# Kernel optimization log

Measured on AMD Instinct MI355X. Metric: run time of the kernel, lower is better.

The kernel has to match this reference:

```python
import jax, jax.numpy as jnp
import numpy as np

VOCAB, ENC, DEC, ATT, EMB = 10000, 2048, 512, 512, 512
B, P, L = 64, 196, 20


def setup_inputs() -> dict:
    key = jax.random.key(0)
    ks = jax.random.split(key, 24)
    s = lambda k, shape, fan: jax.random.normal(k, shape, jnp.float32) / np.sqrt(fan)
    inp = {
        "img_features": jax.random.normal(ks[0], (B, P, ENC), jnp.float32),
        "captions": jax.random.randint(ks[1], (B, L), 0, VOCAB),
        # init-state projections
        "W_init_h": s(ks[2], (DEC, ENC), ENC), "b_init_h": jnp.zeros((DEC,), jnp.float32),
        "W_init_c": s(ks[3], (DEC, ENC), ENC), "b_init_c": jnp.zeros((DEC,), jnp.float32),
        # attention
        "W_dec": s(ks[4], (ATT, DEC), DEC), "b_dec": jnp.zeros((ATT,), jnp.float32),
        "W_enc": s(ks[5], (ATT, ENC), ENC), "b_enc": jnp.zeros((ATT,), jnp.float32),
        "W_fin": s(ks[6], (1, ATT), ATT), "b_fin": jnp.zeros((1,), jnp.float32),
        # gate + output + embedding
        "W_gate": s(ks[7], (ENC, DEC), DEC), "b_gate": jnp.zeros((ENC,), jnp.float32),
        "W_out": s(ks[8], (VOCAB, DEC), DEC), "b_out": jnp.zeros((VOCAB,), jnp.float32),
        "emb": s(ks[9], (VOCAB, EMB), EMB),
        # LSTMCell (PyTorch gate order: i, f, g, o)
        "W_ih": s(ks[10], (4 * DEC, EMB + ENC), EMB + ENC), "b_ih": jnp.zeros((4 * DEC,), jnp.float32),
        "W_hh": s(ks[11], (4 * DEC, DEC), DEC), "b_hh": jnp.zeros((4 * DEC,), jnp.float32),
    }
    return inp


def _decode(img_features, captions, W_init_h, b_init_h, W_init_c, b_init_c,
            W_dec, b_dec, W_enc, b_enc, W_fin, b_fin,
            W_gate, b_gate, W_out, b_out, emb, W_ih, W_hh, b_ih, b_hh):
    # lengths are uniform (padded tensor), so sort/restore are identity and
    # batch_size_t == B at every step.
    avg = img_features.mean(axis=1)                              # [B,ENC]
    h0 = jnp.tanh(avg @ W_init_h.T + b_init_h)                   # [B,DEC]
    c0 = jnp.tanh(avg @ W_init_c.T + b_init_c)
    enc_proj = img_features @ W_enc.T + b_enc                    # [B,P,ATT] (loop-invariant)
    emb_seq = emb[captions[:, :-1]]                              # [B,T,EMB], T = L-1

    def step(carry, e_t):
        h, c = carry
        U_h = h @ W_dec.T + b_dec                                # [B,ATT]
        att = jnp.tanh(enc_proj + U_h[:, None, :])               # [B,P,ATT]
        e = (att @ W_fin.T + b_fin)[..., 0]                      # [B,P]
        alpha = jax.nn.softmax(e, axis=1)
        context = jnp.einsum('bpe,bp->be', img_features, alpha)  # [B,ENC]
        gate = jax.nn.sigmoid(h @ W_gate.T + b_gate)             # [B,ENC]
        x = jnp.concatenate([e_t, gate * context], axis=1)       # [B,EMB+ENC]
        gates = x @ W_ih.T + b_ih + h @ W_hh.T + b_hh            # [B,4*DEC]
        i, f, g, o = jnp.split(gates, 4, axis=1)
        c_new = jax.nn.sigmoid(f) * c + jax.nn.sigmoid(i) * jnp.tanh(g)
        h_new = jax.nn.sigmoid(o) * jnp.tanh(c_new)
        out = h_new @ W_out.T + b_out                            # [B,VOCAB] (dropout=eval identity)
        return (h_new, c_new), (out, alpha)

    _, (preds, alphas) = jax.lax.scan(step, (h0, c0), jnp.swapaxes(emb_seq, 0, 1))
    return jnp.swapaxes(preds, 0, 1), jnp.swapaxes(alphas, 0, 1)  # [B,T,VOCAB], [B,T,P]


def reference(img_features, captions, W_init_h, b_init_h, W_init_c, b_init_c,
              W_dec, b_dec, W_enc, b_enc, W_fin, b_fin,
              W_gate, b_gate, W_out, b_out, emb, W_ih, W_hh, b_ih, b_hh):
    return _decode(img_features, captions, W_init_h, b_init_h, W_init_c, b_init_c,
                   W_dec, b_dec, W_enc, b_enc, W_fin, b_fin,
                   W_gate, b_gate, W_out, b_out, emb, W_ih, W_hh, b_ih, b_hh)
```

## Files before the change

kernel.cpp:

```cpp
#include <hip/hip_runtime.h>
#include <hip/hip_bf16.h>

typedef unsigned short u16;
typedef unsigned int   u32;

#define BB    64
#define PP    196
#define ENC   2048
#define DEC   512
#define ATT   512
#define EMB   512
#define VOCAB 10000
#define VPAD  10048
#define TT    19
#define LCAP  20
#define XDIM  3072
#define LDSTR 40
#define LD64  72

typedef __bf16 bf16x8 __attribute__((ext_vector_type(8)));
typedef float  f32x4  __attribute__((ext_vector_type(4)));

__device__ __forceinline__ float bf2f(u16 u) {
  union { float f; u32 i; } v; v.i = ((u32)u) << 16; return v.f;
}
__device__ __forceinline__ u16 f2bf(float f) {
  u32 x = __float_as_uint(f);
  u32 r = (x + 0x7FFFu + ((x >> 16) & 1u)) >> 16;
  return (u16)r;
}
__device__ __forceinline__ u32 pack2(float a, float b) {
  return (u32)f2bf(a) | ((u32)f2bf(b) << 16);
}
__device__ __forceinline__ float wred_sum(float v) {
  #pragma unroll
  for (int off = 32; off > 0; off >>= 1) v += __shfl_xor(v, off, 64);
  return v;
}
__device__ __forceinline__ float wred_max(float v) {
  #pragma unroll
  for (int off = 32; off > 0; off >>= 1) v = fmaxf(v, __shfl_xor(v, off, 64));
  return v;
}
__device__ __forceinline__ float tanh_fast(float x) {
  return 1.f - 2.f / (__expf(2.f * x) + 1.f);
}
__device__ __forceinline__ float sigm(float x) {
  return 1.f / (1.f + __expf(-x));
}

__global__ __launch_bounds__(256) void k_cvt_simple(u16* __restrict__ dst,
    const float* __restrict__ src, int n4) {
  int stride = gridDim.x * blockDim.x;
  for (int i = blockIdx.x * blockDim.x + threadIdx.x; i < n4; i += stride) {
    float4 v = ((const float4*)src)[i];
    ((uint2*)dst)[i] = make_uint2(pack2(v.x, v.y), pack2(v.z, v.w));
  }
}

__global__ __launch_bounds__(256) void k_cvt_pad(u16* __restrict__ dst,
    const float* __restrict__ src) {
  int total = VPAD * (DEC / 2);
  int stride = gridDim.x * blockDim.x;
  for (int i = blockIdx.x * blockDim.x + threadIdx.x; i < total; i += stride) {
    int row = i >> 8, c2 = i & 255;
    u32 v = 0;
    if (row < VOCAB) {
      float2 f = ((const float2*)src)[(size_t)row * 256 + c2];
      v = pack2(f.x, f.y);
    }
    ((u32*)dst)[i] = v;
  }
}

__global__ __launch_bounds__(256) void k_cvt_comb(u16* __restrict__ dst,
    const float* __restrict__ Wih, const float* __restrict__ Whh) {
  int j = blockIdx.x;
  for (int t = threadIdx.x; t < 768; t += 256) {
    int col = t * 4;
    float4 v = (col < 2560)
        ? ((const float4*)(Wih + (size_t)j * 2560))[t]
        : ((const float4*)(Whh + (size_t)j * 512))[(col - 2560) >> 2];
    ((uint2*)(dst + (size_t)j * XDIM))[t] = make_uint2(pack2(v.x, v.y), pack2(v.z, v.w));
  }
}

__global__ __launch_bounds__(256) void k_avg(const float* __restrict__ img,
    u16* __restrict__ avgb) {
  int b = blockIdx.x;
  int col = blockIdx.y * 256 + threadIdx.x;
  const float* base = img + (size_t)b * PP * ENC + col;
  float s = 0.f;
  for (int p = 0; p < PP; ++p) s += base[(size_t)p * ENC];
  avgb[b * ENC + col] = f2bf(s * (1.f / PP));
}

__global__ __launch_bounds__(256) void k_init_mfma(const u16* __restrict__ avgb,
    const u16* __restrict__ Winitb, const float* __restrict__ bh,
    const float* __restrict__ bc, u16* __restrict__ h, float* __restrict__ c) {
  __shared__ __align__(16) u16 As[2 * 64 * LD64];
  __shared__ __align__(16) u16 Bs[2 * 64 * LD64];
  int n0 = blockIdx.x * 64;
  int tid = threadIdx.x, wv = tid >> 6, lane = tid & 63;
  int wm = wv >> 1, wn = wv & 1;
  int fr = lane & 15, kg = (lane >> 4) * 8, rq = lane >> 4;
  int r0 = tid >> 3, kc0 = (tid & 7) * 8;
  int r1 = (tid + 256) >> 3, kc1 = ((tid + 256) & 7) * 8;
  uint4 pa0 = *(const uint4*)&avgb[(size_t)r0 * ENC + kc0];
  uint4 pa1 = *(const uint4*)&avgb[(size_t)r1 * ENC + kc1];
  uint4 pb0 = *(const uint4*)&Winitb[(size_t)(n0 + r0) * ENC + kc0];
  uint4 pb1 = *(const uint4*)&Winitb[(size_t)(n0 + r1) * ENC + kc1];
  f32x4 acc[2][2] = {};
  const int NK = ENC / 64;
  for (int kt = 0; kt < NK; ++kt) {
    u16* as = As + (kt & 1) * (64 * LD64);
    u16* bs = Bs + (kt & 1) * (64 * LD64);
    *(uint4*)&as[r0 * LD64 + kc0] = pa0;
    *(uint4*)&as[r1 * LD64 + kc1] = pa1;
    *(uint4*)&bs[r0 * LD64 + kc0] = pb0;
    *(uint4*)&bs[r1 * LD64 + kc1] = pb1;
    __syncthreads();
    if (kt + 1 < NK) {
      int k0 = (kt + 1) * 64;
      pa0 = *(const uint4*)&avgb[(size_t)r0 * ENC + k0 + kc0];
      pa1 = *(const uint4*)&avgb[(size_t)r1 * ENC + k0 + kc1];
      pb0 = *(const uint4*)&Winitb[(size_t)(n0 + r0) * ENC + k0 + kc0];
      pb1 = *(const uint4*)&Winitb[(size_t)(n0 + r1) * ENC + k0 + kc1];
    }
    #pragma unroll
    for (int ks = 0; ks < 2; ++ks) {
      bf16x8 a0 = *(const bf16x8*)&as[(wm * 32 + fr) * LD64 + ks * 32 + kg];
      bf16x8 a1 = *(const bf16x8*)&as[(wm * 32 + 16 + fr) * LD64 + ks * 32 + kg];
      bf16x8 b0 = *(const bf16x8*)&bs[(wn * 32 + fr) * LD64 + ks * 32 + kg];
      bf16x8 b1 = *(const bf16x8*)&bs[(wn * 32 + 16 + fr) * LD64 + ks * 32 + kg];
      acc[0][0] = __builtin_amdgcn_mfma_f32_16x16x32_bf16(a0, b0, acc[0][0], 0, 0, 0);
      acc[0][1] = __builtin_amdgcn_mfma_f32_16x16x32_bf16(a0, b1, acc[0][1], 0, 0, 0);
      acc[1][0] = __builtin_amdgcn_mfma_f32_16x16x32_bf16(a1, b0, acc[1][0], 0, 0, 0);
      acc[1][1] = __builtin_amdgcn_mfma_f32_16x16x32_bf16(a1, b1, acc[1][1], 0, 0, 0);
    }
  }
  #pragma unroll
  for (int mi = 0; mi < 2; ++mi)
    for (int ni = 0; ni < 2; ++ni)
      #pragma unroll
      for (int r = 0; r < 4; ++r) {
        int m = wm * 32 + mi * 16 + rq * 4 + r;
        int n = n0 + wn * 32 + ni * 16 + fr;
        float v = acc[mi][ni][r];
        if (n < DEC) h[m * DEC + n] = f2bf(tanh_fast(v + bh[n]));
        else         c[m * DEC + (n - DEC)] = tanh_fast(v + bc[n - DEC]);
      }
}

__global__ __launch_bounds__(256) void k_encproj(const float* __restrict__ A,
    const float* __restrict__ Wencf, const float* __restrict__ benc, u16* __restrict__ epj) {
  __shared__ __align__(16) u16 As[128 * LDSTR];
  __shared__ __align__(16) u16 Bs[128 * LDSTR];
  int m0 = blockIdx.x * 128, n0 = blockIdx.y * 128;
  int tid = threadIdx.x, wv = tid >> 6, lane = tid & 63;
  int wm = wv >> 1, wn = wv & 1;
  int fr = lane & 15, kg = (lane >> 4) * 8, rq = lane >> 4;
  f32x4 acc[4][4] = {};
  for (int k0 = 0; k0 < ENC; k0 += 32) {
    __syncthreads();
    #pragma unroll
    for (int i = 0; i < 2; ++i) {
      int id = tid + i * 256;
      int r = id >> 2, kc = id & 3;
      const float* asrc = &A[(size_t)(m0 + r) * ENC + k0 + kc * 8];
      float4 f0 = ((const float4*)asrc)[0];
      float4 f1 = ((const float4*)asrc)[1];
      *(uint4*)(&As[r * LDSTR + kc * 8]) =
          make_uint4(pack2(f0.x, f0.y), pack2(f0.z, f0.w),
                     pack2(f1.x, f1.y), pack2(f1.z, f1.w));
      const float* bsrc = &Wencf[(size_t)(n0 + r) * ENC + k0 + kc * 8];
      float4 g0 = ((const float4*)bsrc)[0];
      float4 g1 = ((const float4*)bsrc)[1];
      *(uint4*)(&Bs[r * LDSTR + kc * 8]) =
          make_uint4(pack2(g0.x, g0.y), pack2(g0.z, g0.w),
                     pack2(g1.x, g1.y), pack2(g1.z, g1.w));
    }
    __syncthreads();
    bf16x8 af[4], bfr[4];
    #pragma unroll
    for (int i = 0; i < 4; ++i) {
      af[i]  = *(const bf16x8*)(&As[(wm * 64 + i * 16 + fr) * LDSTR + kg]);
      bfr[i] = *(const bf16x8*)(&Bs[(wn * 64 + i * 16 + fr) * LDSTR + kg]);
    }
    #pragma unroll
    for (int mi = 0; mi < 4; ++mi)
      #pragma unroll
      for (int ni = 0; ni < 4; ++ni)
        acc[mi][ni] = __builtin_amdgcn_mfma_f32_16x16x32_bf16(af[mi], bfr[ni], acc[mi][ni], 0, 0, 0);
  }
  #pragma unroll
  for (int mi = 0; mi < 4; ++mi)
    for (int ni = 0; ni < 4; ++ni)
      #pragma unroll
      for (int r = 0; r < 4; ++r) {
        int m = m0 + wm * 64 + mi * 16 + rq * 4 + r;
        int n = n0 + wn * 64 + ni * 16 + fr;
        epj[(size_t)m * ATT + n] = f2bf(acc[mi][ni][r] + benc[n]);
      }
}

__global__ __launch_bounds__(256) void k_hcons(const u16* __restrict__ h,
    const u16* __restrict__ Wdecb, const float* __restrict__ bdec,
    const u16* __restrict__ Wgateb, const float* __restrict__ bgate,
    const u16* __restrict__ Woutb, const float* __restrict__ bout,
    float* __restrict__ uh, float* __restrict__ gate,
    float* __restrict__ preds, u16* __restrict__ x, int step) {
  __shared__ __align__(16) u16 As[2 * 64 * LD64];
  __shared__ __align__(16) u16 Bs[2 * 64 * LD64];
  int bid = blockIdx.x;
  int tid = threadIdx.x, wv = tid >> 6, lane = tid & 63;
  int wm = wv >> 1, wn = wv & 1;
  int fr = lane & 15, kg = (lane >> 4) * 8, rq = lane >> 4;

  if (bid == 0) {
    for (int i = tid; i < 16384; i += 256) {
      int b = i >> 8, jp = (i & 255) * 2;
      *(u32*)(&x[(size_t)b * XDIM + 2560 + jp]) = *(const u32*)(&h[b * DEC + jp]);
    }
  }

  int role, nt; const u16* Wsrc;
  if (bid < 8)       { role = 0; nt = bid;      Wsrc = Wdecb;  }
  else if (bid < 40) { role = 1; nt = bid - 8;  Wsrc = Wgateb; }
  else               { role = 2; nt = bid - 40; Wsrc = Woutb;  }
  int n0 = nt * 64;

  int r0 = tid >> 3, kc0 = (tid & 7) * 8;
  int r1 = (tid + 256) >> 3, kc1 = ((tid + 256) & 7) * 8;
  uint4 pa0 = *(const uint4*)&h[(size_t)r0 * DEC + kc0];
  uint4 pa1 = *(const uint4*)&h[(size_t)r1 * DEC + kc1];
  uint4 pb0 = *(const uint4*)&Wsrc[(size_t)(n0 + r0) * DEC + kc0];
  uint4 pb1 = *(const uint4*)&Wsrc[(size_t)(n0 + r1) * DEC + kc1];
  f32x4 acc[2][2] = {};
  const int NK = DEC / 64;
  for (int kt = 0; kt < NK; ++kt) {
    u16* as = As + (kt & 1) * (64 * LD64);
    u16* bs = Bs + (kt & 1) * (64 * LD64);
    *(uint4*)&as[r0 * LD64 + kc0] = pa0;
    *(uint4*)&as[r1 * LD64 + kc1] = pa1;
    *(uint4*)&bs[r0 * LD64 + kc0] = pb0;
    *(uint4*)&bs[r1 * LD64 + kc1] = pb1;
    __syncthreads();
    if (kt + 1 < NK) {
      int k0 = (kt + 1) * 64;
      pa0 = *(const uint4*)&h[(size_t)r0 * DEC + k0 + kc0];
      pa1 = *(const uint4*)&h[(size_t)r1 * DEC + k0 + kc1];
      pb0 = *(const uint4*)&Wsrc[(size_t)(n0 + r0) * DEC + k0 + kc0];
      pb1 = *(const uint4*)&Wsrc[(size_t)(n0 + r1) * DEC + k0 + kc1];
    }
    #pragma unroll
    for (int ks = 0; ks < 2; ++ks) {
      bf16x8 a0 = *(const bf16x8*)&as[(wm * 32 + fr) * LD64 + ks * 32 + kg];
      bf16x8 a1 = *(const bf16x8*)&as[(wm * 32 + 16 + fr) * LD64 + ks * 32 + kg];
      bf16x8 b0 = *(const bf16x8*)&bs[(wn * 32 + fr) * LD64 + ks * 32 + kg];
      bf16x8 b1 = *(const bf16x8*)&bs[(wn * 32 + 16 + fr) * LD64 + ks * 32 + kg];
      acc[0][0] = __builtin_amdgcn_mfma_f32_16x16x32_bf16(a0, b0, acc[0][0], 0, 0, 0);
      acc[0][1] = __builtin_amdgcn_mfma_f32_16x16x32_bf16(a0, b1, acc[0][1], 0, 0, 0);
      acc[1][0] = __builtin_amdgcn_mfma_f32_16x16x32_bf16(a1, b0, acc[1][0], 0, 0, 0);
      acc[1][1] = __builtin_amdgcn_mfma_f32_16x16x32_bf16(a1, b1, acc[1][1], 0, 0, 0);
    }
  }
  #pragma unroll
  for (int mi = 0; mi < 2; ++mi)
    for (int ni = 0; ni < 2; ++ni)
      #pragma unroll
      for (int r = 0; r < 4; ++r) {
        int m = wm * 32 + mi * 16 + rq * 4 + r;
        int n = n0 + wn * 32 + ni * 16 + fr;
        float v = acc[mi][ni][r];
        if (role == 0) {
          uh[m * DEC + n] = v + bdec[n];
        } else if (role == 1) {
          gate[m * ENC + n] = sigm(v + bgate[n]);
        } else if (n < VOCAB) {
          preds[(size_t)m * (TT * VOCAB) + (size_t)step * VOCAB + n] = v + bout[n];
        }
      }
}

__global__ __launch_bounds__(256) void k_escore(const float* __restrict__ uh,
    const u16* __restrict__ epj, const float* __restrict__ wfin, const float* __restrict__ bfin,
    const int* __restrict__ captions, const float* __restrict__ emb,
    float* __restrict__ e_ws, u16* __restrict__ x, int step) {
  __shared__ float s_uh[ATT], s_wf[ATT];
  int b = blockIdx.x, pt = blockIdx.y;
  int tid = threadIdx.x;
  for (int i = tid; i < ATT; i += 256) { s_uh[i] = uh[b * ATT + i]; s_wf[i] = wfin[i]; }
  __syncthreads();
  if (pt == 0) {
    int capv = captions[b * LCAP + step];
    float2 f = ((const float2*)(emb + (size_t)capv * EMB))[tid];
    ((u32*)(x + (size_t)b * XDIM))[tid] = pack2(f.x, f.y);
  }
  int w = tid >> 6, lane = tid & 63;
  float b0 = bfin[0];
  for (int pl = w; pl < 49; pl += 4) {
    int p = pt * 49 + pl;
    const u16* row = epj + (size_t)(b * PP + p) * ATT;
    float acc = 0.f;
    #pragma unroll
    for (int ki = 0; ki < 8; ++ki) {
      int a = lane + ki * 64;
      acc += tanh_fast(bf2f(row[a]) + s_uh[a]) * s_wf[a];
    }
    acc = wred_sum(acc);
    if (lane == 0) e_ws[b * PP + p] = acc + b0;
  }
}

template <int SRC>
__global__ __launch_bounds__(256) void k_ctx(const float* __restrict__ e_ws,
    const float* __restrict__ gate, const u16* __restrict__ imgb,
    const float* __restrict__ imgf,
    u16* __restrict__ x, float* __restrict__ alphas, int step) {
  __shared__ float s_a[PP];
  int b = blockIdx.x, et = blockIdx.y;
  int tid = threadIdx.x;
  if (tid < PP) s_a[tid] = e_ws[b * PP + tid];
  __syncthreads();
  if (tid < 64) {
    float v0 = s_a[tid], v1 = s_a[tid + 64], v2 = s_a[tid + 128];
    float v3 = (tid + 192 < PP) ? s_a[tid + 192] : -1e30f;
    float m = wred_max(fmaxf(fmaxf(v0, v1), fmaxf(v2, v3)));
    float e0 = __expf(v0 - m), e1 = __expf(v1 - m), e2 = __expf(v2 - m);
    float e3 = (tid + 192 < PP) ? __expf(v3 - m) : 0.f;
    float inv = 1.f / wred_sum(e0 + e1 + e2 + e3);
    s_a[tid] = e0 * inv; s_a[tid + 64] = e1 * inv; s_a[tid + 128] = e2 * inv;
    if (tid + 192 < PP) s_a[tid + 192] = e3 * inv;
  }
  __syncthreads();
  if (et == 0 && tid < PP)
    alphas[(size_t)b * (TT * PP) + (size_t)step * PP + tid] = s_a[tid];
  int e0i = et * 512 + tid * 2;
  float c0 = 0.f, c1 = 0.f;
  if (SRC == 0) {
    const u16* ib = imgb + (size_t)b * PP * ENC + e0i;
    for (int p = 0; p < PP; ++p) {
      u32 v = *(const u32*)(ib + (size_t)p * ENC);
      float ap = s_a[p];
      c0 += ap * bf2f((u16)(v & 0xFFFF));
      c1 += ap * bf2f((u16)(v >> 16));
    }
  } else {
    const float* ib = imgf + (size_t)b * PP * ENC + e0i;
    for (int p = 0; p < PP; ++p) {
      float2 v = *(const float2*)(ib + (size_t)p * ENC);
      float ap = s_a[p];
      c0 += ap * v.x;
      c1 += ap * v.y;
    }
  }
  float g0 = gate[b * ENC + e0i], g1 = gate[b * ENC + e0i + 1];
  *(u32*)(&x[(size_t)b * XDIM + 512 + e0i]) = pack2(c0 * g0, c1 * g1);
}

__global__ __launch_bounds__(256) void k_lstm_part(const u16* __restrict__ x,
    const u16* __restrict__ Wcomb, float* __restrict__ pbuf) {
  __shared__ __align__(16) u16 As[2 * 64 * LD64];
  __shared__ __align__(16) u16 Bs[2 * 64 * LD64];
  int jt = blockIdx.x, ksp = blockIdx.y;
  int kbase = ksp * 768;
  int tid = threadIdx.x, wv = tid >> 6, lane = tid & 63;
  int wm = wv >> 1, wn = wv & 1;
  int fr = lane & 15, kg = (lane >> 4) * 8, rq = lane >> 4;
  int r0 = tid >> 3, kc0 = (tid & 7) * 8;
  int r1 = (tid + 256) >> 3, kc1 = ((tid + 256) & 7) * 8;
  int wrow0 = (r0 >> 4) * 512 + jt * 16 + (r0 & 15);
  int wrow1 = (r1 >> 4) * 512 + jt * 16 + (r1 & 15);
  uint4 pa0 = *(const uint4*)&x[(size_t)r0 * XDIM + kbase + kc0];
  uint4 pa1 = *(const uint4*)&x[(size_t)r1 * XDIM + kbase + kc1];
  uint4 pb0 = *(const uint4*)&Wcomb[(size_t)wrow0 * XDIM + kbase + kc0];
  uint4 pb1 = *(const uint4*)&Wcomb[(size_t)wrow1 * XDIM + kbase + kc1];
  f32x4 acc[2][2] = {};
  const int NK = 12;
  for (int kt = 0; kt < NK; ++kt) {
    u16* as = As + (kt & 1) * (64 * LD64);
    u16* bs = Bs + (kt & 1) * (64 * LD64);
    *(uint4*)&as[r0 * LD64 + kc0] = pa0;
    *(uint4*)&as[r1 * LD64 + kc1] = pa1;
    *(uint4*)&bs[r0 * LD64 + kc0] = pb0;
    *(uint4*)&bs[r1 * LD64 + kc1] = pb1;
    __syncthreads();
    if (kt + 1 < NK) {
      int k0 = kbase + (kt + 1) * 64;
      pa0 = *(const uint4*)&x[(size_t)r0 * XDIM + k0 + kc0];
      pa1 = *(const uint4*)&x[(size_t)r1 * XDIM + k0 + kc1];
      pb0 = *(const uint4*)&Wcomb[(size_t)wrow0 * XDIM + k0 + kc0];
      pb1 = *(const uint4*)&Wcomb[(size_t)wrow1 * XDIM + k0 + kc1];
    }
    #pragma unroll
    for (int ks = 0; ks < 2; ++ks) {
      bf16x8 a0 = *(const bf16x8*)&as[(wm * 32 + fr) * LD64 + ks * 32 + kg];
      bf16x8 a1 = *(const bf16x8*)&as[(wm * 32 + 16 + fr) * LD64 + ks * 32 + kg];
      bf16x8 b0 = *(const bf16x8*)&bs[(wn * 32 + fr) * LD64 + ks * 32 + kg];
      bf16x8 b1 = *(const bf16x8*)&bs[(wn * 32 + 16 + fr) * LD64 + ks * 32 + kg];
      acc[0][0] = __builtin_amdgcn_mfma_f32_16x16x32_bf16(a0, b0, acc[0][0], 0, 0, 0);
      acc[0][1] = __builtin_amdgcn_mfma_f32_16x16x32_bf16(a0, b1, acc[0][1], 0, 0, 0);
      acc[1][0] = __builtin_amdgcn_mfma_f32_16x16x32_bf16(a1, b0, acc[1][0], 0, 0, 0);
      acc[1][1] = __builtin_amdgcn_mfma_f32_16x16x32_bf16(a1, b1, acc[1][1], 0, 0, 0);
    }
  }
  float* pout = pbuf + (size_t)(ksp * 32 + jt) * 4096;
  #pragma unroll
  for (int mi = 0; mi < 2; ++mi)
    for (int ni = 0; ni < 2; ++ni)
      #pragma unroll
      for (int r = 0; r < 4; ++r) {
        int m = wm * 32 + mi * 16 + rq * 4 + r;
        int n = wn * 32 + ni * 16 + fr;
        pout[m * 64 + n] = acc[mi][ni][r];
      }
}

__global__ __launch_bounds__(256) void k_lstm_fin(const float* __restrict__ pbuf,
    const float* __restrict__ bih, const float* __restrict__ bhh,
    float* __restrict__ c, u16* __restrict__ h) {
  int jt = blockIdx.x, tid = threadIdx.x;
  #pragma unroll
  for (int ii = 0; ii < 4; ++ii) {
    int idx = tid + ii * 256;
    int bb = idx >> 4, jj = idx & 15;
    int j = jt * 16 + jj;
    float g4[4];
    #pragma unroll
    for (int g = 0; g < 4; ++g) {
      float s = 0.f;
      #pragma unroll
      for (int ks = 0; ks < 4; ++ks)
        s += pbuf[(size_t)(ks * 32 + jt) * 4096 + bb * 64 + g * 16 + jj];
      g4[g] = s;
    }
    float iv = g4[0] + bih[j]        + bhh[j];
    float fv = g4[1] + bih[512 + j]  + bhh[512 + j];
    float gv = g4[2] + bih[1024 + j] + bhh[1024 + j];
    float ov = g4[3] + bih[1536 + j] + bhh[1536 + j];
    float co = c[bb * DEC + j];
    float cn = sigm(fv) * co + sigm(iv) * tanh_fast(gv);
    float hn = sigm(ov) * tanh_fast(cn);
    c[bb * DEC + j] = cn;
    h[bb * DEC + j] = f2bf(hn);
  }
}

extern "C" void kernel_launch(void* const* d_in, const int* in_sizes, int n_in,
                              void* d_out, int out_size, void* d_ws, size_t ws_size,
                              hipStream_t stream) {
  const float* img   = (const float*)d_in[0];
  const int*   cap   = (const int*)  d_in[1];
  const float* Winh  = (const float*)d_in[2];
  const float* binh  = (const float*)d_in[3];
  const float* Winc  = (const float*)d_in[4];
  const float* binc  = (const float*)d_in[5];
  const float* Wdec  = (const float*)d_in[6];
  const float* bdec  = (const float*)d_in[7];
  const float* Wenc  = (const float*)d_in[8];
  const float* benc  = (const float*)d_in[9];
  const float* Wfin  = (const float*)d_in[10];
  const float* bfin  = (const float*)d_in[11];
  const float* Wgate = (const float*)d_in[12];
  const float* bgate = (const float*)d_in[13];
  const float* Wout  = (const float*)d_in[14];
  const float* bout  = (const float*)d_in[15];
  const float* emb   = (const float*)d_in[16];
  const float* Wih   = (const float*)d_in[17];
  const float* bih   = (const float*)d_in[18];
  const float* Whh   = (const float*)d_in[19];
  const float* bhh   = (const float*)d_in[20];

  char* ws = (char*)d_ws;
  u16*   epj    = (u16*)  (ws);
  u16*   Winitb = (u16*)  (ws);
  u16*   avgb   = (u16*)  (ws + 4194304);
  u16*   Wcomb  = (u16*)  (ws + 12845056);
  u16*   Woutb  = (u16*)  (ws + 25427968);
  u16*   Wgateb = (u16*)  (ws + 35717120);
  u16*   Wdecb  = (u16*)  (ws + 37814272);
  float* pbuf   = (float*)(ws + 38338560);
  u16*   h      = (u16*)  (ws + 40435712);
  float* c      = (float*)(ws + 40501248);
  float* e_ws   = (float*)(ws + 40632320);
  u16*   x      = (u16*)  (ws + 40683520);
  float* uh     = (float*)(ws + 41076736);
  float* gate   = (float*)(ws + 41207808);
  u16*   imgb   = (u16*)  (ws + 41732096);
  const bool use_imgb = (ws_size >= 93112320ull);

  float* preds  = (float*)d_out;
  float* alphas = (float*)d_out + (size_t)BB * TT * VOCAB;

  k_cvt_simple<<<512,  256, 0, stream>>>(Winitb,                Winh, 262144);
  k_cvt_simple<<<512,  256, 0, stream>>>(Winitb + 512 * ENC,    Winc, 262144);
  if (use_imgb)
    k_cvt_simple<<<4096, 256, 0, stream>>>(imgb, img, 6422528);
  k_cvt_simple<<<512,  256, 0, stream>>>(Wgateb, Wgate, 262144);
  k_cvt_simple<<<128,  256, 0, stream>>>(Wdecb,  Wdec,  65536);
  k_cvt_pad   <<<2048, 256, 0, stream>>>(Woutb,  Wout);
  k_cvt_comb  <<<2048, 256, 0, stream>>>(Wcomb,  Wih, Whh);

  k_avg<<<dim3(BB, 8), 256, 0, stream>>>(img, avgb);
  k_init_mfma<<<16, 256, 0, stream>>>(avgb, Winitb, binh, binc, h, c);
  k_encproj<<<dim3(98, 4), 256, 0, stream>>>(img, Wenc, benc, epj);
  k_hcons<<<40, 256, 0, stream>>>(h, Wdecb, bdec, Wgateb, bgate, Woutb, bout,
                                  uh, gate, nullptr, x, 0);
  for (int t = 0; t < TT; ++t) {
    k_escore<<<dim3(BB, 4), 256, 0, stream>>>(uh, epj, Wfin, bfin, cap, emb, e_ws, x, t);
    if (use_imgb)
      k_ctx<0><<<dim3(BB, 4), 256, 0, stream>>>(e_ws, gate, imgb, img, x, alphas, t);
    else
      k_ctx<1><<<dim3(BB, 4), 256, 0, stream>>>(e_ws, gate, imgb, img, x, alphas, t);
    k_lstm_part<<<dim3(32, 4), 256, 0, stream>>>(x, Wcomb, pbuf);
    k_lstm_fin<<<32, 256, 0, stream>>>(pbuf, bih, bhh, c, h);
    k_hcons<<<197, 256, 0, stream>>>(h, Wdecb, bdec, Wgateb, bgate, Woutb, bout,
                                     uh, gate, preds, x, t);
  }
}
```

Measured before the change: 1.200 ms.

## Fuse attention score and context kernels, fold LSTM finalize via atomic counter

Merges the per-step score kernel and the softmax/context kernel into one 512-thread block per batch row, keeping scores in shared memory instead of a workspace round trip. The LSTM partial-sum kernel now finishes its own reduction: the last of the four split-K blocks, found with an atomic counter, applies the gate nonlinearities. Together these drop two launches per step. The encoder projection also reads pre-converted bf16 image and weight buffers. The trade-off is fewer blocks per attention launch (64 instead of 256) and threadfence/atomic synchronisation in the LSTM kernel.

```diff
diff --git a/kernel.cpp b/kernel.cpp
--- a/kernel.cpp
+++ b/kernel.cpp
@@ -48,6 +48,8 @@
 __device__ __forceinline__ float sigm(float x) {
   return 1.f / (1.f + __expf(-x));
 }
+
+__global__ void k_zero(u32* __restrict__ p) { p[threadIdx.x] = 0; }
 
 __global__ __launch_bounds__(256) void k_cvt_simple(u16* __restrict__ dst,
     const float* __restrict__ src, int n4) {
@@ -152,8 +154,11 @@
       }
 }
 
-__global__ __launch_bounds__(256) void k_encproj(const float* __restrict__ A,
-    const float* __restrict__ Wencf, const float* __restrict__ benc, u16* __restrict__ epj) {
+template <int SRC>
+__global__ __launch_bounds__(256) void k_encproj(
+    const u16* __restrict__ Ab, const float* __restrict__ Af,
+    const u16* __restrict__ Wb, const float* __restrict__ Wf,
+    const float* __restrict__ benc, u16* __restrict__ epj) {
   __shared__ __align__(16) u16 As[128 * LDSTR];
   __shared__ __align__(16) u16 Bs[128 * LDSTR];
   int m0 = blockIdx.x * 128, n0 = blockIdx.y * 128;
@@ -167,18 +172,23 @@
     for (int i = 0; i < 2; ++i) {
       int id = tid + i * 256;
       int r = id >> 2, kc = id & 3;
-      const float* asrc = &A[(size_t)(m0 + r) * ENC + k0 + kc * 8];
-      float4 f0 = ((const float4*)asrc)[0];
-      float4 f1 = ((const float4*)asrc)[1];
-      *(uint4*)(&As[r * LDSTR + kc * 8]) =
-          make_uint4(pack2(f0.x, f0.y), pack2(f0.z, f0.w),
-                     pack2(f1.x, f1.y), pack2(f1.z, f1.w));
-      const float* bsrc = &Wencf[(size_t)(n0 + r) * ENC + k0 + kc * 8];
-      float4 g0 = ((const float4*)bsrc)[0];
-      float4 g1 = ((const float4*)bsrc)[1];
-      *(uint4*)(&Bs[r * LDSTR + kc * 8]) =
-          make_uint4(pack2(g0.x, g0.y), pack2(g0.z, g0.w),
-                     pack2(g1.x, g1.y), pack2(g1.z, g1.w));
+      if (SRC == 0) {
+        *(uint4*)(&As[r * LDSTR + kc * 8]) = *(const uint4*)(&Ab[(size_t)(m0 + r) * ENC + k0 + kc * 8]);
+        *(uint4*)(&Bs[r * LDSTR + kc * 8]) = *(const uint4*)(&Wb[(size_t)(n0 + r) * ENC + k0 + kc * 8]);
+      } else {
+        const float* asrc = &Af[(size_t)(m0 + r) * ENC + k0 + kc * 8];
+        float4 f0 = ((const float4*)asrc)[0];
+        float4 f1 = ((const float4*)asrc)[1];
+        *(uint4*)(&As[r * LDSTR + kc * 8]) =
+            make_uint4(pack2(f0.x, f0.y), pack2(f0.z, f0.w),
+                       pack2(f1.x, f1.y), pack2(f1.z, f1.w));
+        const float* bsrc = &Wf[(size_t)(n0 + r) * ENC + k0 + kc * 8];
+        float4 g0 = ((const float4*)bsrc)[0];
+        float4 g1 = ((const float4*)bsrc)[1];
+        *(uint4*)(&Bs[r * LDSTR + kc * 8]) =
+            make_uint4(pack2(g0.x, g0.y), pack2(g0.z, g0.w),
+                       pack2(g1.x, g1.y), pack2(g1.z, g1.w));
+      }
     }
     __syncthreads();
     bf16x8 af[4], bfr[4];
@@ -283,24 +293,26 @@
       }
 }
 
-__global__ __launch_bounds__(256) void k_escore(const float* __restrict__ uh,
+template <int SRC>
+__global__ __launch_bounds__(512) void k_att(const float* __restrict__ uh,
     const u16* __restrict__ epj, const float* __restrict__ wfin, const float* __restrict__ bfin,
     const int* __restrict__ captions, const float* __restrict__ emb,
-    float* __restrict__ e_ws, u16* __restrict__ x, int step) {
+    const float* __restrict__ gate, const u16* __restrict__ imgb,
+    const float* __restrict__ imgf,
+    u16* __restrict__ x, float* __restrict__ alphas, int step) {
   __shared__ float s_uh[ATT], s_wf[ATT];
-  int b = blockIdx.x, pt = blockIdx.y;
-  int tid = threadIdx.x;
-  for (int i = tid; i < ATT; i += 256) { s_uh[i] = uh[b * ATT + i]; s_wf[i] = wfin[i]; }
-  __syncthreads();
-  if (pt == 0) {
+  __shared__ float s_e[PP];
+  int b = blockIdx.x;
+  int tid = threadIdx.x, wv = tid >> 6, lane = tid & 63;
+  if (tid < ATT) { s_uh[tid] = uh[b * ATT + tid]; s_wf[tid] = wfin[tid]; }
+  if (tid < 256) {
     int capv = captions[b * LCAP + step];
     float2 f = ((const float2*)(emb + (size_t)capv * EMB))[tid];
     ((u32*)(x + (size_t)b * XDIM))[tid] = pack2(f.x, f.y);
   }
-  int w = tid >> 6, lane = tid & 63;
+  __syncthreads();
   float b0 = bfin[0];
-  for (int pl = w; pl < 49; pl += 4) {
-    int p = pt * 49 + pl;
+  for (int p = wv; p < PP; p += 8) {
     const u16* row = epj + (size_t)(b * PP + p) * ATT;
     float acc = 0.f;
     #pragma unroll
@@ -309,60 +321,55 @@
       acc += tanh_fast(bf2f(row[a]) + s_uh[a]) * s_wf[a];
     }
     acc = wred_sum(acc);
-    if (lane == 0) e_ws[b * PP + p] = acc + b0;
-  }
-}
-
-template <int SRC>
-__global__ __launch_bounds__(256) void k_ctx(const float* __restrict__ e_ws,
-    const float* __restrict__ gate, const u16* __restrict__ imgb,
-    const float* __restrict__ imgf,
-    u16* __restrict__ x, float* __restrict__ alphas, int step) {
-  __shared__ float s_a[PP];
-  int b = blockIdx.x, et = blockIdx.y;
-  int tid = threadIdx.x;
-  if (tid < PP) s_a[tid] = e_ws[b * PP + tid];
+    if (lane == 0) s_e[p] = acc + b0;
+  }
   __syncthreads();
   if (tid < 64) {
-    float v0 = s_a[tid], v1 = s_a[tid + 64], v2 = s_a[tid + 128];
-    float v3 = (tid + 192 < PP) ? s_a[tid + 192] : -1e30f;
+    float v0 = s_e[tid], v1 = s_e[tid + 64], v2 = s_e[tid + 128];
+    float v3 = (tid + 192 < PP) ? s_e[tid + 192] : -1e30f;
     float m = wred_max(fmaxf(fmaxf(v0, v1), fmaxf(v2, v3)));
     float e0 = __expf(v0 - m), e1 = __expf(v1 - m), e2 = __expf(v2 - m);
     float e3 = (tid + 192 < PP) ? __expf(v3 - m) : 0.f;
     float inv = 1.f / wred_sum(e0 + e1 + e2 + e3);
-    s_a[tid] = e0 * inv; s_a[tid + 64] = e1 * inv; s_a[tid + 128] = e2 * inv;
-    if (tid + 192 < PP) s_a[tid + 192] = e3 * inv;
+    s_e[tid] = e0 * inv; s_e[tid + 64] = e1 * inv; s_e[tid + 128] = e2 * inv;
+    if (tid + 192 < PP) s_e[tid + 192] = e3 * inv;
   }
   __syncthreads();
-  if (et == 0 && tid < PP)
-    alphas[(size_t)b * (TT * PP) + (size_t)step * PP + tid] = s_a[tid];
-  int e0i = et * 512 + tid * 2;
-  float c0 = 0.f, c1 = 0.f;
+  if (tid < PP)
+    alphas[(size_t)b * (TT * PP) + (size_t)step * PP + tid] = s_e[tid];
+  int e0i = tid * 4;
+  float c0 = 0.f, c1 = 0.f, c2 = 0.f, c3 = 0.f;
   if (SRC == 0) {
     const u16* ib = imgb + (size_t)b * PP * ENC + e0i;
     for (int p = 0; p < PP; ++p) {
-      u32 v = *(const u32*)(ib + (size_t)p * ENC);
-      float ap = s_a[p];
-      c0 += ap * bf2f((u16)(v & 0xFFFF));
-      c1 += ap * bf2f((u16)(v >> 16));
+      uint2 v = *(const uint2*)(ib + (size_t)p * ENC);
+      float ap = s_e[p];
+      c0 += ap * bf2f((u16)(v.x & 0xFFFF));
+      c1 += ap * bf2f((u16)(v.x >> 16));
+      c2 += ap * bf2f((u16)(v.y & 0xFFFF));
+      c3 += ap * bf2f((u16)(v.y >> 16));
     }
   } else {
     const float* ib = imgf + (size_t)b * PP * ENC + e0i;
     for (int p = 0; p < PP; ++p) {
-      float2 v = *(const float2*)(ib + (size_t)p * ENC);
-      float ap = s_a[p];
-      c0 += ap * v.x;
-      c1 += ap * v.y;
-    }
-  }
-  float g0 = gate[b * ENC + e0i], g1 = gate[b * ENC + e0i + 1];
-  *(u32*)(&x[(size_t)b * XDIM + 512 + e0i]) = pack2(c0 * g0, c1 * g1);
-}
-
-__global__ __launch_bounds__(256) void k_lstm_part(const u16* __restrict__ x,
-    const u16* __restrict__ Wcomb, float* __restrict__ pbuf) {
+      float4 v = *(const float4*)(ib + (size_t)p * ENC);
+      float ap = s_e[p];
+      c0 += ap * v.x; c1 += ap * v.y; c2 += ap * v.z; c3 += ap * v.w;
+    }
+  }
+  float4 g = *(const float4*)(&gate[b * ENC + e0i]);
+  ((uint2*)(x + (size_t)b * XDIM + 512))[tid] =
+      make_uint2(pack2(c0 * g.x, c1 * g.y), pack2(c2 * g.z, c3 * g.w));
+}
+
+__global__ __launch_bounds__(256) void k_lstm(const u16* __restrict__ x,
+    const u16* __restrict__ Wcomb,
+    const float* __restrict__ bih, const float* __restrict__ bhh,
+    float* __restrict__ c, u16* __restrict__ h,
+    float* __restrict__ pbuf, u32* __restrict__ ctr) {
   __shared__ __align__(16) u16 As[2 * 64 * LD64];
   __shared__ __align__(16) u16 Bs[2 * 64 * LD64];
+  __shared__ u32 s_last;
   int jt = blockIdx.x, ksp = blockIdx.y;
   int kbase = ksp * 768;
   int tid = threadIdx.x, wv = tid >> 6, lane = tid & 63;
@@ -415,35 +422,40 @@
         int n = wn * 32 + ni * 16 + fr;
         pout[m * 64 + n] = acc[mi][ni][r];
       }
-}
-
-__global__ __launch_bounds__(256) void k_lstm_fin(const float* __restrict__ pbuf,
-    const float* __restrict__ bih, const float* __restrict__ bhh,
-    float* __restrict__ c, u16* __restrict__ h) {
-  int jt = blockIdx.x, tid = threadIdx.x;
-  #pragma unroll
-  for (int ii = 0; ii < 4; ++ii) {
-    int idx = tid + ii * 256;
-    int bb = idx >> 4, jj = idx & 15;
-    int j = jt * 16 + jj;
-    float g4[4];
-    #pragma unroll
-    for (int g = 0; g < 4; ++g) {
-      float s = 0.f;
+  __threadfence();
+  __syncthreads();
+  if (tid == 0) {
+    u32 old = atomicAdd(&ctr[jt], 1);
+    s_last = (old == 3) ? 1u : 0u;
+  }
+  __syncthreads();
+  if (s_last) {
+    __threadfence();
+    #pragma unroll
+    for (int ii = 0; ii < 4; ++ii) {
+      int idx = tid + ii * 256;
+      int bb = idx >> 4, jj = idx & 15;
+      int j = jt * 16 + jj;
+      float g4[4];
       #pragma unroll
-      for (int ks = 0; ks < 4; ++ks)
-        s += pbuf[(size_t)(ks * 32 + jt) * 4096 + bb * 64 + g * 16 + jj];
-      g4[g] = s;
-    }
-    float iv = g4[0] + bih[j]        + bhh[j];
-    float fv = g4[1] + bih[512 + j]  + bhh[512 + j];
-    float gv = g4[2] + bih[1024 + j] + bhh[1024 + j];
-    float ov = g4[3] + bih[1536 + j] + bhh[1536 + j];
-    float co = c[bb * DEC + j];
-    float cn = sigm(fv) * co + sigm(iv) * tanh_fast(gv);
-    float hn = sigm(ov) * tanh_fast(cn);
-    c[bb * DEC + j] = cn;
-    h[bb * DEC + j] = f2bf(hn);
+      for (int g = 0; g < 4; ++g) {
+        float s = 0.f;
+        #pragma unroll
+        for (int ks = 0; ks < 4; ++ks)
+          s += pbuf[(size_t)(ks * 32 + jt) * 4096 + bb * 64 + g * 16 + jj];
+        g4[g] = s;
+      }
+      float iv = g4[0] + bih[j]        + bhh[j];
+      float fv = g4[1] + bih[512 + j]  + bhh[512 + j];
+      float gv = g4[2] + bih[1024 + j] + bhh[1024 + j];
+      float ov = g4[3] + bih[1536 + j] + bhh[1536 + j];
+      float co = c[bb * DEC + j];
+      float cn = sigm(fv) * co + sigm(iv) * tanh_fast(gv);
+      float hn = sigm(ov) * tanh_fast(cn);
+      c[bb * DEC + j] = cn;
+      h[bb * DEC + j] = f2bf(hn);
+    }
+    if (tid == 0) atomicExch(&ctr[jt], 0);
   }
 }
 
@@ -480,23 +492,27 @@
   u16*   Woutb  = (u16*)  (ws + 25427968);
   u16*   Wgateb = (u16*)  (ws + 35717120);
   u16*   Wdecb  = (u16*)  (ws + 37814272);
-  float* pbuf   = (float*)(ws + 38338560);
-  u16*   h      = (u16*)  (ws + 40435712);
-  float* c      = (float*)(ws + 40501248);
-  float* e_ws   = (float*)(ws + 40632320);
-  u16*   x      = (u16*)  (ws + 40683520);
-  float* uh     = (float*)(ws + 41076736);
-  float* gate   = (float*)(ws + 41207808);
-  u16*   imgb   = (u16*)  (ws + 41732096);
-  const bool use_imgb = (ws_size >= 93112320ull);
+  u16*   Wencb  = (u16*)  (ws + 38338560);
+  float* pbuf   = (float*)(ws + 40435712);
+  u32*   ctr    = (u32*)  (ws + 42532864);
+  u16*   h      = (u16*)  (ws + 42533376);
+  float* c      = (float*)(ws + 42598912);
+  u16*   x      = (u16*)  (ws + 42729984);
+  float* uh     = (float*)(ws + 43123200);
+  float* gate   = (float*)(ws + 43254272);
+  u16*   imgb   = (u16*)  (ws + 43778560);
+  const bool use_imgb = (ws_size >= 95158784ull);
 
   float* preds  = (float*)d_out;
   float* alphas = (float*)d_out + (size_t)BB * TT * VOCAB;
 
-  k_cvt_simple<<<512,  256, 0, stream>>>(Winitb,                Winh, 262144);
-  k_cvt_simple<<<512,  256, 0, stream>>>(Winitb + 512 * ENC,    Winc, 262144);
-  if (use_imgb)
-    k_cvt_simple<<<4096, 256, 0, stream>>>(imgb, img, 6422528);
+  k_zero<<<1, 128, 0, stream>>>(ctr);
+  k_cvt_simple<<<512,  256, 0, stream>>>(Winitb,             Winh, 262144);
+  k_cvt_simple<<<512,  256, 0, stream>>>(Winitb + 512 * ENC, Winc, 262144);
+  if (use_imgb) {
+    k_cvt_simple<<<4096, 256, 0, stream>>>(imgb,  img,  6422528);
+    k_cvt_simple<<<512,  256, 0, stream>>>(Wencb, Wenc, 262144);
+  }
   k_cvt_simple<<<512,  256, 0, stream>>>(Wgateb, Wgate, 262144);
   k_cvt_simple<<<128,  256, 0, stream>>>(Wdecb,  Wdec,  65536);
   k_cvt_pad   <<<2048, 256, 0, stream>>>(Woutb,  Wout);
@@ -504,17 +520,18 @@
 
   k_avg<<<dim3(BB, 8), 256, 0, stream>>>(img, avgb);
   k_init_mfma<<<16, 256, 0, stream>>>(avgb, Winitb, binh, binc, h, c);
-  k_encproj<<<dim3(98, 4), 256, 0, stream>>>(img, Wenc, benc, epj);
+  if (use_imgb)
+    k_encproj<0><<<dim3(98, 4), 256, 0, stream>>>(imgb, img, Wencb, Wenc, benc, epj);
+  else
+    k_encproj<1><<<dim3(98, 4), 256, 0, stream>>>(imgb, img, Wencb, Wenc, benc, epj);
   k_hcons<<<40, 256, 0, stream>>>(h, Wdecb, bdec, Wgateb, bgate, Woutb, bout,
                                   uh, gate, nullptr, x, 0);
   for (int t = 0; t < TT; ++t) {
-    k_escore<<<dim3(BB, 4), 256, 0, stream>>>(uh, epj, Wfin, bfin, cap, emb, e_ws, x, t);
     if (use_imgb)
-      k_ctx<0><<<dim3(BB, 4), 256, 0, stream>>>(e_ws, gate, imgb, img, x, alphas, t);
+      k_att<0><<<BB, 512, 0, stream>>>(uh, epj, Wfin, bfin, cap, emb, gate, imgb, img, x, alphas, t);
     else
-      k_ctx<1><<<dim3(BB, 4), 256, 0, stream>>>(e_ws, gate, imgb, img, x, alphas, t);
-    k_lstm_part<<<dim3(32, 4), 256, 0, stream>>>(x, Wcomb, pbuf);
-    k_lstm_fin<<<32, 256, 0, stream>>>(pbuf, bih, bhh, c, h);
+      k_att<1><<<BB, 512, 0, stream>>>(uh, epj, Wfin, bfin, cap, emb, gate, imgb, img, x, alphas, t);
+    k_lstm<<<dim3(32, 4), 256, 0, stream>>>(x, Wcomb, bih, bhh, c, h, pbuf, ctr);
     k_hcons<<<197, 256, 0, stream>>>(h, Wdecb, bdec, Wgateb, bgate, Woutb, bout,
                                      uh, gate, preds, x, t);
   }
```

Result: slower. 1.671 ms (+39.2%).

## Hoist vocab projection out of recurrence into one batched logits GEMM

Applied to the files above, without the earlier changes.

Each step's bf16 hidden state is saved into a history buffer. The per-step output projection (157 of the 197 blocks of k_hcons) is removed from the recurrent loop and replaced by one 128x128-tile MFMA GEMM over all 19x64 rows after the loop, with W_out padded to a multiple of 128 rows. The trailing k_hcons launch at the last step is also skipped. Separately, the encoder projection now reads pre-converted bf16 image and W_enc instead of converting fp32 on the fly. This adds a W_enc conversion pass and a larger workspace, and the logits GEMM reads padded history rows that are uninitialized but masked on output.

```diff
diff --git a/kernel.cpp b/kernel.cpp
--- a/kernel.cpp
+++ b/kernel.cpp
@@ -11,9 +11,10 @@
 #define ATT   512
 #define EMB   512
 #define VOCAB 10000
-#define VPAD  10048
+#define VPAD2 10112
 #define TT    19
 #define LCAP  20
+#define MALL  1280
 #define XDIM  3072
 #define LDSTR 40
 #define LD64  72
@@ -60,7 +61,7 @@
 
 __global__ __launch_bounds__(256) void k_cvt_pad(u16* __restrict__ dst,
     const float* __restrict__ src) {
-  int total = VPAD * (DEC / 2);
+  int total = VPAD2 * (DEC / 2);
   int stride = gridDim.x * blockDim.x;
   for (int i = blockIdx.x * blockDim.x + threadIdx.x; i < total; i += stride) {
     int row = i >> 8, c2 = i & 255;
@@ -152,8 +153,11 @@
       }
 }
 
-__global__ __launch_bounds__(256) void k_encproj(const float* __restrict__ A,
-    const float* __restrict__ Wencf, const float* __restrict__ benc, u16* __restrict__ epj) {
+template <int SRC>
+__global__ __launch_bounds__(256) void k_encproj(
+    const u16* __restrict__ Ab, const float* __restrict__ Af,
+    const u16* __restrict__ Wb, const float* __restrict__ Wf,
+    const float* __restrict__ benc, u16* __restrict__ epj) {
   __shared__ __align__(16) u16 As[128 * LDSTR];
   __shared__ __align__(16) u16 Bs[128 * LDSTR];
   int m0 = blockIdx.x * 128, n0 = blockIdx.y * 128;
@@ -167,18 +171,23 @@
     for (int i = 0; i < 2; ++i) {
       int id = tid + i * 256;
       int r = id >> 2, kc = id & 3;
-      const float* asrc = &A[(size_t)(m0 + r) * ENC + k0 + kc * 8];
-      float4 f0 = ((const float4*)asrc)[0];
-      float4 f1 = ((const float4*)asrc)[1];
-      *(uint4*)(&As[r * LDSTR + kc * 8]) =
-          make_uint4(pack2(f0.x, f0.y), pack2(f0.z, f0.w),
-                     pack2(f1.x, f1.y), pack2(f1.z, f1.w));
-      const float* bsrc = &Wencf[(size_t)(n0 + r) * ENC + k0 + kc * 8];
-      float4 g0 = ((const float4*)bsrc)[0];
-      float4 g1 = ((const float4*)bsrc)[1];
-      *(uint4*)(&Bs[r * LDSTR + kc * 8]) =
-          make_uint4(pack2(g0.x, g0.y), pack2(g0.z, g0.w),
-                     pack2(g1.x, g1.y), pack2(g1.z, g1.w));
+      if (SRC == 0) {
+        *(uint4*)(&As[r * LDSTR + kc * 8]) = *(const uint4*)(&Ab[(size_t)(m0 + r) * ENC + k0 + kc * 8]);
+        *(uint4*)(&Bs[r * LDSTR + kc * 8]) = *(const uint4*)(&Wb[(size_t)(n0 + r) * ENC + k0 + kc * 8]);
+      } else {
+        const float* asrc = &Af[(size_t)(m0 + r) * ENC + k0 + kc * 8];
+        float4 f0 = ((const float4*)asrc)[0];
+        float4 f1 = ((const float4*)asrc)[1];
+        *(uint4*)(&As[r * LDSTR + kc * 8]) =
+            make_uint4(pack2(f0.x, f0.y), pack2(f0.z, f0.w),
+                       pack2(f1.x, f1.y), pack2(f1.z, f1.w));
+        const float* bsrc = &Wf[(size_t)(n0 + r) * ENC + k0 + kc * 8];
+        float4 g0 = ((const float4*)bsrc)[0];
+        float4 g1 = ((const float4*)bsrc)[1];
+        *(uint4*)(&Bs[r * LDSTR + kc * 8]) =
+            make_uint4(pack2(g0.x, g0.y), pack2(g0.z, g0.w),
+                       pack2(g1.x, g1.y), pack2(g1.z, g1.w));
+      }
     }
     __syncthreads();
     bf16x8 af[4], bfr[4];
@@ -204,12 +213,56 @@
       }
 }
 
+__global__ __launch_bounds__(256) void k_logits(const u16* __restrict__ hall,
+    const u16* __restrict__ Woutb2, const float* __restrict__ bout,
+    float* __restrict__ preds) {
+  __shared__ __align__(16) u16 As[128 * LDSTR];
+  __shared__ __align__(16) u16 Bs[128 * LDSTR];
+  int m0 = blockIdx.x * 128, n0 = blockIdx.y * 128;
+  int tid = threadIdx.x, wv = tid >> 6, lane = tid & 63;
+  int wm = wv >> 1, wn = wv & 1;
+  int fr = lane & 15, kg = (lane >> 4) * 8, rq = lane >> 4;
+  f32x4 acc[4][4] = {};
+  for (int k0 = 0; k0 < DEC; k0 += 32) {
+    __syncthreads();
+    #pragma unroll
+    for (int i = 0; i < 2; ++i) {
+      int id = tid + i * 256;
+      int r = id >> 2, kc = id & 3;
+      *(uint4*)(&As[r * LDSTR + kc * 8]) = *(const uint4*)(&hall[(size_t)(m0 + r) * DEC + k0 + kc * 8]);
+      *(uint4*)(&Bs[r * LDSTR + kc * 8]) = *(const uint4*)(&Woutb2[(size_t)(n0 + r) * DEC + k0 + kc * 8]);
+    }
+    __syncthreads();
+    bf16x8 af[4], bfr[4];
+    #pragma unroll
+    for (int i = 0; i < 4; ++i) {
+      af[i]  = *(const bf16x8*)(&As[(wm * 64 + i * 16 + fr) * LDSTR + kg]);
+      bfr[i] = *(const bf16x8*)(&Bs[(wn * 64 + i * 16 + fr) * LDSTR + kg]);
+    }
+    #pragma unroll
+    for (int mi = 0; mi < 4; ++mi)
+      #pragma unroll
+      for (int ni = 0; ni < 4; ++ni)
+        acc[mi][ni] = __builtin_amdgcn_mfma_f32_16x16x32_bf16(af[mi], bfr[ni], acc[mi][ni], 0, 0, 0);
+  }
+  #pragma unroll
+  for (int mi = 0; mi < 4; ++mi)
+    for (int ni = 0; ni < 4; ++ni)
+      #pragma unroll
+      for (int r = 0; r < 4; ++r) {
+        int m = m0 + wm * 64 + mi * 16 + rq * 4 + r;
+        int n = n0 + wn * 64 + ni * 16 + fr;
+        if (m < TT * BB && n < VOCAB) {
+          int t = m >> 6, b = m & 63;
+          preds[(size_t)b * (TT * VOCAB) + (size_t)t * VOCAB + n] = acc[mi][ni][r] + bout[n];
+        }
+      }
+}
+
 __global__ __launch_bounds__(256) void k_hcons(const u16* __restrict__ h,
     const u16* __restrict__ Wdecb, const float* __restrict__ bdec,
     const u16* __restrict__ Wgateb, const float* __restrict__ bgate,
-    const u16* __restrict__ Woutb, const float* __restrict__ bout,
-    float* __restrict__ uh, float* __restrict__ gate,
-    float* __restrict__ preds, u16* __restrict__ x, int step) {
+    float* __restrict__ uh, float* __restrict__ gate, u16* __restrict__ x) {
   __shared__ __align__(16) u16 As[2 * 64 * LD64];
   __shared__ __align__(16) u16 Bs[2 * 64 * LD64];
   int bid = blockIdx.x;
@@ -225,9 +278,8 @@
   }
 
   int role, nt; const u16* Wsrc;
-  if (bid < 8)       { role = 0; nt = bid;      Wsrc = Wdecb;  }
-  else if (bid < 40) { role = 1; nt = bid - 8;  Wsrc = Wgateb; }
-  else               { role = 2; nt = bid - 40; Wsrc = Woutb;  }
+  if (bid < 8) { role = 0; nt = bid;     Wsrc = Wdecb;  }
+  else         { role = 1; nt = bid - 8; Wsrc = Wgateb; }
   int n0 = nt * 64;
 
   int r0 = tid >> 3, kc0 = (tid & 7) * 8;
@@ -273,13 +325,8 @@
         int m = wm * 32 + mi * 16 + rq * 4 + r;
         int n = n0 + wn * 32 + ni * 16 + fr;
         float v = acc[mi][ni][r];
-        if (role == 0) {
-          uh[m * DEC + n] = v + bdec[n];
-        } else if (role == 1) {
-          gate[m * ENC + n] = sigm(v + bgate[n]);
-        } else if (n < VOCAB) {
-          preds[(size_t)m * (TT * VOCAB) + (size_t)step * VOCAB + n] = v + bout[n];
-        }
+        if (role == 0) uh[m * DEC + n] = v + bdec[n];
+        else           gate[m * ENC + n] = sigm(v + bgate[n]);
       }
 }
 
@@ -419,7 +466,7 @@
 
 __global__ __launch_bounds__(256) void k_lstm_fin(const float* __restrict__ pbuf,
     const float* __restrict__ bih, const float* __restrict__ bhh,
-    float* __restrict__ c, u16* __restrict__ h) {
+    float* __restrict__ c, u16* __restrict__ h, u16* __restrict__ hall, int step) {
   int jt = blockIdx.x, tid = threadIdx.x;
   #pragma unroll
   for (int ii = 0; ii < 4; ++ii) {
@@ -443,7 +490,9 @@
     float cn = sigm(fv) * co + sigm(iv) * tanh_fast(gv);
     float hn = sigm(ov) * tanh_fast(cn);
     c[bb * DEC + j] = cn;
-    h[bb * DEC + j] = f2bf(hn);
+    u16 hb = f2bf(hn);
+    h[bb * DEC + j] = hb;
+    hall[(size_t)(step * BB + bb) * DEC + j] = hb;
   }
 }
 
@@ -477,36 +526,42 @@
   u16*   Winitb = (u16*)  (ws);
   u16*   avgb   = (u16*)  (ws + 4194304);
   u16*   Wcomb  = (u16*)  (ws + 12845056);
-  u16*   Woutb  = (u16*)  (ws + 25427968);
-  u16*   Wgateb = (u16*)  (ws + 35717120);
-  u16*   Wdecb  = (u16*)  (ws + 37814272);
-  float* pbuf   = (float*)(ws + 38338560);
-  u16*   h      = (u16*)  (ws + 40435712);
-  float* c      = (float*)(ws + 40501248);
-  float* e_ws   = (float*)(ws + 40632320);
-  u16*   x      = (u16*)  (ws + 40683520);
-  float* uh     = (float*)(ws + 41076736);
-  float* gate   = (float*)(ws + 41207808);
-  u16*   imgb   = (u16*)  (ws + 41732096);
-  const bool use_imgb = (ws_size >= 93112320ull);
+  u16*   Woutb2 = (u16*)  (ws + 25427968);
+  u16*   Wgateb = (u16*)  (ws + 35782656);
+  u16*   Wdecb  = (u16*)  (ws + 37879808);
+  u16*   Wencb  = (u16*)  (ws + 38404096);
+  float* pbuf   = (float*)(ws + 40501248);
+  u16*   h      = (u16*)  (ws + 42598400);
+  float* c      = (float*)(ws + 42663936);
+  float* e_ws   = (float*)(ws + 42795008);
+  u16*   x      = (u16*)  (ws + 42846208);
+  float* uh     = (float*)(ws + 43239424);
+  float* gate   = (float*)(ws + 43370496);
+  u16*   hall   = (u16*)  (ws + 43894784);
+  u16*   imgb   = (u16*)  (ws + 45205504);
+  const bool use_imgb = (ws_size >= 96585728ull);
 
   float* preds  = (float*)d_out;
   float* alphas = (float*)d_out + (size_t)BB * TT * VOCAB;
 
-  k_cvt_simple<<<512,  256, 0, stream>>>(Winitb,                Winh, 262144);
-  k_cvt_simple<<<512,  256, 0, stream>>>(Winitb + 512 * ENC,    Winc, 262144);
-  if (use_imgb)
-    k_cvt_simple<<<4096, 256, 0, stream>>>(imgb, img, 6422528);
+  k_cvt_simple<<<512,  256, 0, stream>>>(Winitb,             Winh, 262144);
+  k_cvt_simple<<<512,  256, 0, stream>>>(Winitb + 512 * ENC, Winc, 262144);
+  if (use_imgb) {
+    k_cvt_simple<<<4096, 256, 0, stream>>>(imgb,  img,  6422528);
+    k_cvt_simple<<<512,  256, 0, stream>>>(Wencb, Wenc, 262144);
+  }
   k_cvt_simple<<<512,  256, 0, stream>>>(Wgateb, Wgate, 262144);
   k_cvt_simple<<<128,  256, 0, stream>>>(Wdecb,  Wdec,  65536);
-  k_cvt_pad   <<<2048, 256, 0, stream>>>(Woutb,  Wout);
+  k_cvt_pad   <<<2048, 256, 0, stream>>>(Woutb2, Wout);
   k_cvt_comb  <<<2048, 256, 0, stream>>>(Wcomb,  Wih, Whh);
 
   k_avg<<<dim3(BB, 8), 256, 0, stream>>>(img, avgb);
   k_init_mfma<<<16, 256, 0, stream>>>(avgb, Winitb, binh, binc, h, c);
-  k_encproj<<<dim3(98, 4), 256, 0, stream>>>(img, Wenc, benc, epj);
-  k_hcons<<<40, 256, 0, stream>>>(h, Wdecb, bdec, Wgateb, bgate, Woutb, bout,
-                                  uh, gate, nullptr, x, 0);
+  if (use_imgb)
+    k_encproj<0><<<dim3(98, 4), 256, 0, stream>>>(imgb, img, Wencb, Wenc, benc, epj);
+  else
+    k_encproj<1><<<dim3(98, 4), 256, 0, stream>>>(imgb, img, Wencb, Wenc, benc, epj);
+  k_hcons<<<40, 256, 0, stream>>>(h, Wdecb, bdec, Wgateb, bgate, uh, gate, x);
   for (int t = 0; t < TT; ++t) {
     k_escore<<<dim3(BB, 4), 256, 0, stream>>>(uh, epj, Wfin, bfin, cap, emb, e_ws, x, t);
     if (use_imgb)
@@ -514,8 +569,9 @@
     else
       k_ctx<1><<<dim3(BB, 4), 256, 0, stream>>>(e_ws, gate, imgb, img, x, alphas, t);
     k_lstm_part<<<dim3(32, 4), 256, 0, stream>>>(x, Wcomb, pbuf);
-    k_lstm_fin<<<32, 256, 0, stream>>>(pbuf, bih, bhh, c, h);
-    k_hcons<<<197, 256, 0, stream>>>(h, Wdecb, bdec, Wgateb, bgate, Woutb, bout,
-                                     uh, gate, preds, x, t);
-  }
-}
+    k_lstm_fin<<<32, 256, 0, stream>>>(pbuf, bih, bhh, c, h, hall, t);
+    if (t + 1 < TT)
+      k_hcons<<<40, 256, 0, stream>>>(h, Wdecb, bdec, Wgateb, bgate, uh, gate, x);
+  }
+  k_logits<<<dim3(10, 79), 256, 0, stream>>>(hall, Woutb2, bout, preds);
+}
```

Result: no change. 1.200 ms (-0.0%).
